# Optimization experiments

Measured on AMD Instinct MI355X. Metric: run time of the kernel, lower is better.

Reference implementation:

```python
import jax, jax.numpy as jnp
import numpy as np

D_MODEL = 1024
NUM_HEADS = 16


def setup_inputs() -> dict:
    key = jax.random.key(0)
    ks = jax.random.split(key, 5)
    scale = 1.0 / np.sqrt(D_MODEL)
    X = jax.random.normal(ks[0], (4, 2048, D_MODEL), dtype=jnp.float32)
    W_q = jax.random.normal(ks[1], (D_MODEL, D_MODEL), dtype=jnp.float32) * scale
    W_k = jax.random.normal(ks[2], (D_MODEL, D_MODEL), dtype=jnp.float32) * scale
    W_v = jax.random.normal(ks[3], (D_MODEL, D_MODEL), dtype=jnp.float32) * scale
    W_o = jax.random.normal(ks[4], (D_MODEL, D_MODEL), dtype=jnp.float32) * scale
    return {"X": X, "W_q": W_q, "W_k": W_k, "W_v": W_v, "W_o": W_o}


def reference(X, W_q, W_k, W_v, W_o):
    b, s, d_model = X.shape
    h = NUM_HEADS
    d_k = d_model // h
    # Linear projections (y = x @ W^T convention; W stored as [out,in] would be
    # x @ W.T, but with random weights we use x @ W — math is identical in form).
    def split_heads(y):
        return y.reshape(b, s, h, d_k).transpose(0, 2, 1, 3)  # b h s d
    q = split_heads(X @ W_q)
    k = split_heads(X @ W_k)
    v = split_heads(X @ W_v)
    scores = jnp.einsum('bhid,bhjd->bhij', q, k) / jnp.sqrt(jnp.float32(d_k))
    causal = jnp.tril(jnp.ones((s, s), dtype=bool))
    scores = jnp.where(causal[None, None], scores, jnp.float32(-jnp.inf))
    probs = jax.nn.softmax(scores, axis=-1)
    attended = jnp.einsum('bhij,bhjd->bhid', probs, v)
    out = attended.transpose(0, 2, 1, 3).reshape(b, s, d_model)
    return out @ W_o
```

## Files before the change

kernel.cpp:

```cpp
#include <hip/hip_runtime.h>

typedef __bf16 bf16;
typedef __attribute__((ext_vector_type(8))) __bf16 bf16x8;
typedef __attribute__((ext_vector_type(4))) float f32x4;
typedef __attribute__((ext_vector_type(16))) float f32x16;
typedef __attribute__((ext_vector_type(4))) unsigned short u16x4;
typedef __attribute__((ext_vector_type(2))) int v2i;

#define D_MODEL 1024
#define SEQ     2048
#define NB      4
#define NH      16
#define DK      64
#define MROWS   (NB * SEQ)

#define MFMA_BF16 __builtin_amdgcn_mfma_f32_16x16x32_bf16
#define MFMA32    __builtin_amdgcn_mfma_f32_32x32x16_bf16
#define EXP2F(x) __builtin_amdgcn_exp2f(x)
#define QSCALE 0.18033688011112042f

__device__ __forceinline__ bf16 f2b(float f) {
    union { float f; unsigned u; } c; c.f = f;
    unsigned r = (c.u + 0x7fffu + ((c.u >> 16) & 1u)) >> 16;
    union { unsigned short s; bf16 b; } o; o.s = (unsigned short)r;
    return o.b;
}
__device__ __forceinline__ unsigned short f2u(float f) {
    union { float f; unsigned u; } c; c.f = f;
    return (unsigned short)((c.u + 0x7fffu + ((c.u >> 16) & 1u)) >> 16);
}

__device__ __forceinline__ f32x16 zero16() {
    f32x16 z = {0.f,0.f,0.f,0.f,0.f,0.f,0.f,0.f,
                0.f,0.f,0.f,0.f,0.f,0.f,0.f,0.f};
    return z;
}

template <int N> struct IC { static constexpr int v = N; };

__global__ void prep_kernel(const float* __restrict__ X,
                            const float* __restrict__ Wq, const float* __restrict__ Wk,
                            const float* __restrict__ Wv, const float* __restrict__ Wo,
                            bf16* __restrict__ Xb, bf16* __restrict__ WqkvT,
                            bf16* __restrict__ WoT) {
    __shared__ float tile[32][33];
    const int bid = blockIdx.x;
    if (bid < 8192) {
        int i = bid * 256 + threadIdx.x;
        float4 v = ((const float4*)X)[i];
        u16x4 o; o[0] = f2u(v.x); o[1] = f2u(v.y); o[2] = f2u(v.z); o[3] = f2u(v.w);
        ((u16x4*)Xb)[i] = o;
    } else {
        int r = bid - 8192;
        int w = r >> 10, tl = r & 1023;
        const float* src = (w == 0) ? Wq : (w == 1) ? Wk : (w == 2) ? Wv : Wo;
        bf16* dst = (w == 3) ? WoT : WqkvT + (size_t)w * 1024 * 1024;
        const int n0 = (tl & 31) * 32, k0 = (tl >> 5) * 32;
        const int tx = threadIdx.x & 31, ty = threadIdx.x >> 5;
#pragma unroll
        for (int i = 0; i < 4; i++)
            tile[ty + i * 8][tx] = src[(size_t)(k0 + ty + i * 8) * 1024 + n0 + tx];
        __syncthreads();
#pragma unroll
        for (int i = 0; i < 4; i++)
            dst[(size_t)(n0 + ty + i * 8) * 1024 + k0 + tx] = f2b(tile[tx][ty + i * 8]);
    }
}

__global__ __launch_bounds__(256) void gemm_qkv(const bf16* __restrict__ A,
                                                const bf16* __restrict__ Bt,
                                                bf16* __restrict__ outQ,
                                                bf16* __restrict__ outV) {
    __shared__ __align__(16) bf16 lA[128 * 64];
    __shared__ __align__(16) bf16 lB[128 * 64];

    const int t = threadIdx.x;
    const int wid = t >> 6, lane = t & 63;
    const int ln = lane & 15, qd = lane >> 4;
    const int wm = wid >> 1, wn = wid & 1;

    const int bid = blockIdx.x;
    const int idx = bid >> 3;
    const int colb = (bid & 7) * 3 + (idx % 3);
    const int rowb = idx / 3;
    const int row0 = rowb * 128, col0 = colb * 128;
    const bool isQK = (col0 < 2048);

    const int srow = t >> 3;
    const int schunk = (t & 7) ^ (srow & 7);
    const bf16* ga = A  + (size_t)(row0 + srow) * 1024 + schunk * 8;
    const bf16* gb = Bt + (size_t)(col0 + srow) * 1024 + schunk * 8;
    const int swk = ln & 7;

    f32x4 acc[4][4];
#pragma unroll
    for (int i = 0; i < 4; i++)
#pragma unroll
        for (int j = 0; j < 4; j++) acc[i][j] = (f32x4){0.f, 0.f, 0.f, 0.f};

    for (int kb = 0; kb < 1024; kb += 64) {
#pragma unroll
        for (int c = 0; c < 4; c++) {
            __builtin_amdgcn_global_load_lds(
                (const __attribute__((address_space(1))) void*)(ga + kb + (size_t)c * 32 * 1024),
                (__attribute__((address_space(3))) void*)(&lA[t * 8 + c * 2048]), 16, 0, 0);
            __builtin_amdgcn_global_load_lds(
                (const __attribute__((address_space(1))) void*)(gb + kb + (size_t)c * 32 * 1024),
                (__attribute__((address_space(3))) void*)(&lB[t * 8 + c * 2048]), 16, 0, 0);
        }
        __syncthreads();

#pragma unroll
        for (int ks = 0; ks < 2; ks++) {
            bf16x8 af[4], bfr[4];
#pragma unroll
            for (int i = 0; i < 4; i++)
                af[i] = *(const bf16x8*)&lA[(wm * 64 + i * 16 + ln) * 64
                                            + ((ks * 4 + qd) ^ swk) * 8];
#pragma unroll
            for (int j = 0; j < 4; j++)
                bfr[j] = *(const bf16x8*)&lB[(wn * 64 + j * 16 + ln) * 64
                                             + ((ks * 4 + qd) ^ swk) * 8];
            if (isQK) {
#pragma unroll
                for (int i = 0; i < 4; i++)
#pragma unroll
                    for (int j = 0; j < 4; j++)
                        acc[i][j] = MFMA_BF16(bfr[j], af[i], acc[i][j], 0, 0, 0);
            } else {
#pragma unroll
                for (int i = 0; i < 4; i++)
#pragma unroll
                    for (int j = 0; j < 4; j++)
                        acc[i][j] = MFMA_BF16(af[i], bfr[j], acc[i][j], 0, 0, 0);
            }
        }
        __syncthreads();
    }

    if (isQK) {
#pragma unroll
        for (int i = 0; i < 4; i++)
#pragma unroll
            for (int j = 0; j < 4; j++) {
                int m  = row0 + wm * 64 + i * 16 + ln;
                int n0 = col0 + wn * 64 + j * 16 + qd * 4;
                float scale = (n0 < 1024) ? QSCALE : 1.0f;
                int b = m >> 11, s = m & 2047;
                int h = (n0 & 1023) >> 6, d0 = n0 & 63;
                size_t addr = (((size_t)(b * NH + h) * SEQ + s) * DK + d0)
                              + (size_t)(n0 >> 10) * 8388608;
                u16x4 w;
#pragma unroll
                for (int r = 0; r < 4; r++) w[r] = f2u(acc[i][j][r] * scale);
                *(u16x4*)&outQ[addr] = w;
            }
    } else {
#pragma unroll
        for (int i = 0; i < 4; i++)
#pragma unroll
            for (int j = 0; j < 4; j++) {
                int m0 = row0 + wm * 64 + i * 16 + qd * 4;
                int n  = col0 + wn * 64 + j * 16 + ln - 2048;
                int b = m0 >> 11, s0 = m0 & 2047;
                int h = n >> 6, d = n & 63;
                size_t addr = ((size_t)(b * NH + h) * DK + d) * SEQ + s0;
                u16x4 w;
#pragma unroll
                for (int r = 0; r < 4; r++) w[r] = f2u(acc[i][j][r]);
                *(u16x4*)&outV[addr] = w;
            }
    }
}

__global__ __launch_bounds__(256) void gemm_o(const bf16* __restrict__ A,
                                              const bf16* __restrict__ Bt,
                                              float* __restrict__ out) {
    __shared__ __align__(16) bf16 lA[128 * 64];
    __shared__ __align__(16) bf16 lB[128 * 64];

    const int t = threadIdx.x;
    const int wid = t >> 6, lane = t & 63;
    const int ln = lane & 15, qd = lane >> 4;
    const int wm = wid >> 1, wn = wid & 1;

    const int bid = blockIdx.x;
    const int colb = bid & 7, rowb = bid >> 3;
    const int row0 = rowb * 128, col0 = colb * 128;

    const int srow = t >> 3;
    const int schunk = (t & 7) ^ (srow & 7);
    const bf16* ga = A  + (size_t)(row0 + srow) * 1024 + schunk * 8;
    const bf16* gb = Bt + (size_t)(col0 + srow) * 1024 + schunk * 8;
    const int swk = ln & 7;

    f32x4 acc[4][4];
#pragma unroll
    for (int i = 0; i < 4; i++)
#pragma unroll
        for (int j = 0; j < 4; j++) acc[i][j] = (f32x4){0.f, 0.f, 0.f, 0.f};

    for (int kb = 0; kb < 1024; kb += 64) {
#pragma unroll
        for (int c = 0; c < 4; c++) {
            __builtin_amdgcn_global_load_lds(
                (const __attribute__((address_space(1))) void*)(ga + kb + (size_t)c * 32 * 1024),
                (__attribute__((address_space(3))) void*)(&lA[t * 8 + c * 2048]), 16, 0, 0);
            __builtin_amdgcn_global_load_lds(
                (const __attribute__((address_space(1))) void*)(gb + kb + (size_t)c * 32 * 1024),
                (__attribute__((address_space(3))) void*)(&lB[t * 8 + c * 2048]), 16, 0, 0);
        }
        __syncthreads();

#pragma unroll
        for (int ks = 0; ks < 2; ks++) {
            bf16x8 af[4], bfr[4];
#pragma unroll
            for (int i = 0; i < 4; i++)
                af[i] = *(const bf16x8*)&lA[(wm * 64 + i * 16 + ln) * 64
                                            + ((ks * 4 + qd) ^ swk) * 8];
#pragma unroll
            for (int j = 0; j < 4; j++)
                bfr[j] = *(const bf16x8*)&lB[(wn * 64 + j * 16 + ln) * 64
                                             + ((ks * 4 + qd) ^ swk) * 8];
#pragma unroll
            for (int i = 0; i < 4; i++)
#pragma unroll
                for (int j = 0; j < 4; j++)
                    acc[i][j] = MFMA_BF16(bfr[j], af[i], acc[i][j], 0, 0, 0);
        }
        __syncthreads();
    }

#pragma unroll
    for (int i = 0; i < 4; i++)
#pragma unroll
        for (int j = 0; j < 4; j++) {
            int m  = row0 + wm * 64 + i * 16 + ln;
            int n0 = col0 + wn * 64 + j * 16 + qd * 4;
            *(f32x4*)&out[(size_t)m * 1024 + n0] = acc[i][j];
        }
}

__global__ __launch_bounds__(256, 2) void attn_kernel(const bf16* __restrict__ Q,
                                                      const bf16* __restrict__ K,
                                                      const bf16* __restrict__ Vt,
                                                      bf16* __restrict__ attn_out) {
    __shared__ __align__(16) bf16 smem[4][64 * 64];

    const int t = threadIdx.x;
    const int wid = t >> 6, lane = t & 63;
    const int qcol = lane & 31, h = lane >> 5;

    const int bid = blockIdx.x;
    const int bh = ((bid >> 6) << 3) | (bid & 7);
    const int p  = (bid >> 3) & 7;
    const int gA = 15 - p, gB = p;
    const int ntA = 2 * gA + 2;

    const bf16* Qh = Q  + (size_t)bh * SEQ * DK;
    const bf16* Kh = K  + (size_t)bh * SEQ * DK;
    const bf16* Vh = Vt + (size_t)bh * DK * SEQ;

    const int srow = t >> 3;
    const int schunk = (t & 7) ^ (srow & 7);
    const bf16* kgp = Kh + (size_t)srow * DK + schunk * 8;
    const bf16* vgp = Vh + (size_t)srow * SEQ + schunk * 8;

    const char* sbase = (const char*)&smem[0][0];
    int raddr[4];
#pragma unroll
    for (int tt = 0; tt < 4; tt++)
        raddr[tt] = qcol * 128 + (((2 * tt + h) ^ (lane & 7)) * 16);

    int qw0;
    bf16x8 qf[4];
    f32x16 o[2];
    float l;

    auto initGroup = [&](int g) {
        qw0 = g * 128 + wid * 32;
#pragma unroll
        for (int tt = 0; tt < 4; tt++)
            qf[tt] = *(const bf16x8*)(Qh + (size_t)(qw0 + qcol) * DK + tt * 16 + h * 8);
        o[0] = zero16(); o[1] = zero16();
        l = 0.f;
    };

    const int b = bh >> 4, head = bh & 15;
    auto finalize = [&]() {
        float ll = l + __shfl_xor(l, 32);
        const float inv = 1.0f / ll;
        const size_t orow = ((size_t)(b * SEQ + qw0 + qcol)) * D_MODEL + head * DK;
#pragma unroll
        for (int m = 0; m < 2; m++)
#pragma unroll
            for (int q4 = 0; q4 < 4; q4++) {
                u16x4 w;
#pragma unroll
                for (int c = 0; c < 4; c++) w[c] = f2u(o[m][q4 * 4 + c] * inv);
                *(u16x4*)&attn_out[orow + m * 32 + q4 * 8 + h * 4] = w;
            }
    };

    auto stage = [&](int kb, int buf) {
#pragma unroll
        for (int c = 0; c < 2; c++) {
            __builtin_amdgcn_global_load_lds(
                (const __attribute__((address_space(1))) void*)(kgp + (size_t)(kb + c * 32) * DK),
                (__attribute__((address_space(3))) void*)(&smem[buf][t * 8 + c * 2048]), 16, 0, 0);
            __builtin_amdgcn_global_load_lds(
                (const __attribute__((address_space(1))) void*)(vgp + (size_t)c * 32 * SEQ + kb),
                (__attribute__((address_space(3))) void*)(&smem[2 + buf][t * 8 + c * 2048]), 16, 0, 0);
        }
    };

    auto qkt = [&](const char* kb_base) -> f32x16 {
        f32x16 z = zero16();
#pragma unroll
        for (int tt = 0; tt < 4; tt++) {
            bf16x8 kf = *(const bf16x8*)(kb_base + raddr[tt]);
            z = MFMA32(kf, qf[tt], z, 0, 0, 0);
        }
        return z;
    };

    auto pvks = [&](const f32x16& s, int b8, int ks, const char* vbase) {
        unsigned A, B, C, D;
        asm("v_cvt_pk_bf16_f32 %0, %1, %2"
            : "=v"(A) : "v"(s[b8 + 0]), "v"(s[b8 + 1]));
        asm("v_cvt_pk_bf16_f32 %0, %1, %2"
            : "=v"(B) : "v"(s[b8 + 2]), "v"(s[b8 + 3]));
        asm("v_cvt_pk_bf16_f32 %0, %1, %2"
            : "=v"(C) : "v"(s[b8 + 4]), "v"(s[b8 + 5]));
        asm("v_cvt_pk_bf16_f32 %0, %1, %2"
            : "=v"(D) : "v"(s[b8 + 6]), "v"(s[b8 + 7]));
        v2i r02 = __builtin_amdgcn_permlane32_swap((int)A, (int)C, false, false);
        v2i r13 = __builtin_amdgcn_permlane32_swap((int)B, (int)D, false, false);
        union { unsigned u[4]; bf16x8 v; } pf;
        pf.u[0] = (unsigned)r02[0];
        pf.u[1] = (unsigned)r13[0];
        pf.u[2] = (unsigned)r02[1];
        pf.u[3] = (unsigned)r13[1];
#pragma unroll
        for (int m = 0; m < 2; m++) {
            bf16x8 vf = *(const bf16x8*)(vbase + raddr[ks] + m * 4096);
            o[m] = MFMA32(vf, pf.v, o[m], 0, 0, 0);
        }
    };

    auto smaxFull = [&](f32x16& s) -> float {
#pragma unroll
        for (int r = 0; r < 16; r++) s[r] = EXP2F(s[r]);
        float s0 = (s[0] + s[1]) + (s[2] + s[3]);
        float s1 = (s[4] + s[5]) + (s[6] + s[7]);
        float s2 = (s[8] + s[9]) + (s[10] + s[11]);
        float s3 = (s[12] + s[13]) + (s[14] + s[15]);
        return (s0 + s1) + (s2 + s3);
    };

    auto compute = [&](auto curc, int kb) {
        constexpr int CUR = decltype(curc)::v;
        const char* kbase = sbase + CUR * 8192;
        const char* vbase = sbase + 16384 + CUR * 8192;
        const int rel = qw0 - kb;
        if (rel < 0) return;
        if (rel >= 64) {
            __builtin_amdgcn_s_setprio(1);
            f32x16 s0 = qkt(kbase);
            f32x16 s1 = qkt(kbase + 4096);
            __builtin_amdgcn_s_setprio(0);
            l += smaxFull(s0);
            __builtin_amdgcn_s_setprio(1);
            pvks(s0, 0, 0, vbase);
            pvks(s0, 8, 1, vbase);
            __builtin_amdgcn_s_setprio(0);
            l += smaxFull(s1);
            __builtin_amdgcn_s_setprio(1);
            pvks(s1, 0, 2, vbase);
            pvks(s1, 8, 3, vbase);
            __builtin_amdgcn_s_setprio(0);
        } else {
            const int nt = (rel >> 5) + 1;
            f32x16 st[2];
#pragma unroll
            for (int n = 0; n < 2; n++)
                if (n < nt) st[n] = qkt(kbase + n * 4096);
            float ps = 0.f;
#pragma unroll
            for (int n = 0; n < 2; n++)
                if (n < nt) {
                    const bool diag = (rel == 32 * n);
#pragma unroll
                    for (int r = 0; r < 16; r++) {
                        float pv = EXP2F(st[n][r]);
                        if (diag) {
                            const int kloc = (r & 3) + 8 * (r >> 2) + 4 * h;
                            pv = (kloc > qcol) ? 0.f : pv;
                        }
                        st[n][r] = pv;
                    }
                    float s0 = (st[n][0] + st[n][1]) + (st[n][2] + st[n][3]);
                    float s1 = (st[n][4] + st[n][5]) + (st[n][6] + st[n][7]);
                    float s2 = (st[n][8] + st[n][9]) + (st[n][10] + st[n][11]);
                    float s3 = (st[n][12] + st[n][13]) + (st[n][14] + st[n][15]);
                    ps += (s0 + s1) + (s2 + s3);
                }
            l += ps;
#pragma unroll
            for (int ks = 0; ks < 4; ks++)
                if (ks < 2 * nt)
                    pvks(st[ks >> 1], (ks & 1) * 8, ks, vbase);
        }
    };

    auto step = [&](auto curc, int i) {
        constexpr int CUR = decltype(curc)::v;
        __syncthreads();
        const int nx = i + 1;
        if (nx < 34) {
            const int tnx = (nx < ntA) ? nx : nx - ntA;
            stage(tnx * 64, CUR ^ 1);
        }
        const int kb = ((i < ntA) ? i : i - ntA) * 64;
        compute(curc, kb);
        if (i == ntA - 1) { finalize(); initGroup(gB); }
    };

    stage(0, 0);
    initGroup(gA);

    step(IC<0>{}, 0);
#pragma unroll 1
    for (int ii = 0; ii < 16; ii++) {
        step(IC<1>{}, 2 * ii + 1);
        step(IC<0>{}, 2 * ii + 2);
    }
    step(IC<1>{}, 33);
    finalize();
}

extern "C" void kernel_launch(void* const* d_in, const int* in_sizes, int n_in,
                              void* d_out, int out_size, void* d_ws, size_t ws_size,
                              hipStream_t stream) {
    const float* X  = (const float*)d_in[0];
    const float* Wq = (const float*)d_in[1];
    const float* Wk = (const float*)d_in[2];
    const float* Wv = (const float*)d_in[3];
    const float* Wo = (const float*)d_in[4];
    float* out = (float*)d_out;
    char* ws = (char*)d_ws;

    bf16* Xb    = (bf16*)(ws);
    bf16* WqkvT = (bf16*)(ws + (16u << 20));
    bf16* WoT   = (bf16*)(ws + (22u << 20));
    bf16* Qb    = (bf16*)(ws + (24u << 20));
    bf16* Vt    = (bf16*)(ws + (56u << 20));
    bf16* Attn  = Xb;
    bf16* Kb    = Qb + (size_t)8388608;

    prep_kernel<<<dim3(12288), dim3(256), 0, stream>>>(X, Wq, Wk, Wv, Wo,
                                                       Xb, WqkvT, WoT);

    gemm_qkv<<<dim3(1536), dim3(256), 0, stream>>>(Xb, WqkvT, Qb, Vt);

    attn_kernel<<<dim3(512), dim3(256), 0, stream>>>(Qb, Kb, Vt, Attn);

    gemm_o<<<dim3(512), dim3(256), 0, stream>>>(Attn, WoT, out);
}
```

Baseline: 234.3 us.

## Double attention K/V tile depth to 128 keys per stage, vectorize weight transpose stores

The attention kernel now stages 128 keys per double-buffered step instead of 64. This halves the number of __syncthreads barriers and stage issues across the KV loop, and the shared-memory buffers grow to 64 KB. The 128-key tile is processed as two 64-key halves, with the causal mask handled per half. Separately, the weight-transpose kernel now writes four packed bf16 values per thread as a single 8-byte store instead of four scalar stores. The larger LDS footprint may limit occupancy below the two-blocks-per-CU launch bound, and the diagonal block may now load keys that go unused.

```diff
diff --git a/kernel.cpp b/kernel.cpp
--- a/kernel.cpp
+++ b/kernel.cpp
@@ -61,9 +61,12 @@
         for (int i = 0; i < 4; i++)
             tile[ty + i * 8][tx] = src[(size_t)(k0 + ty + i * 8) * 1024 + n0 + tx];
         __syncthreads();
-#pragma unroll
-        for (int i = 0; i < 4; i++)
-            dst[(size_t)(n0 + ty + i * 8) * 1024 + k0 + tx] = f2b(tile[tx][ty + i * 8]);
+        const int n4 = threadIdx.x >> 3;
+        const int k4 = (threadIdx.x & 7) * 4;
+        u16x4 ww;
+#pragma unroll
+        for (int j = 0; j < 4; j++) ww[j] = f2u(tile[k4 + j][n4]);
+        *(u16x4*)&dst[(size_t)(n0 + n4) * 1024 + k0 + k4] = ww;
     }
 }
 
@@ -246,7 +249,7 @@
                                                       const bf16* __restrict__ K,
                                                       const bf16* __restrict__ Vt,
                                                       bf16* __restrict__ attn_out) {
-    __shared__ __align__(16) bf16 smem[4][64 * 64];
+    __shared__ __align__(16) bf16 smem[4][128 * 64];
 
     const int t = threadIdx.x;
     const int wid = t >> 6, lane = t & 63;
@@ -256,7 +259,7 @@
     const int bh = ((bid >> 6) << 3) | (bid & 7);
     const int p  = (bid >> 3) & 7;
     const int gA = 15 - p, gB = p;
-    const int ntA = 2 * gA + 2;
+    const int ntA = gA + 1;
 
     const bf16* Qh = Q  + (size_t)bh * SEQ * DK;
     const bf16* Kh = K  + (size_t)bh * SEQ * DK;
@@ -305,14 +308,19 @@
 
     auto stage = [&](int kb, int buf) {
 #pragma unroll
-        for (int c = 0; c < 2; c++) {
+        for (int c = 0; c < 4; c++)
             __builtin_amdgcn_global_load_lds(
                 (const __attribute__((address_space(1))) void*)(kgp + (size_t)(kb + c * 32) * DK),
                 (__attribute__((address_space(3))) void*)(&smem[buf][t * 8 + c * 2048]), 16, 0, 0);
-            __builtin_amdgcn_global_load_lds(
-                (const __attribute__((address_space(1))) void*)(vgp + (size_t)c * 32 * SEQ + kb),
-                (__attribute__((address_space(3))) void*)(&smem[2 + buf][t * 8 + c * 2048]), 16, 0, 0);
-        }
+#pragma unroll
+        for (int hh = 0; hh < 2; hh++)
+#pragma unroll
+            for (int c = 0; c < 2; c++)
+                __builtin_amdgcn_global_load_lds(
+                    (const __attribute__((address_space(1))) void*)
+                        (vgp + (size_t)c * 32 * SEQ + kb + hh * 64),
+                    (__attribute__((address_space(3))) void*)
+                        (&smem[2 + buf][t * 8 + hh * 4096 + c * 2048]), 16, 0, 0);
     };
 
     auto qkt = [&](const char* kb_base) -> f32x16 {
@@ -361,56 +369,61 @@
 
     auto compute = [&](auto curc, int kb) {
         constexpr int CUR = decltype(curc)::v;
-        const char* kbase = sbase + CUR * 8192;
-        const char* vbase = sbase + 16384 + CUR * 8192;
-        const int rel = qw0 - kb;
-        if (rel < 0) return;
-        if (rel >= 64) {
-            __builtin_amdgcn_s_setprio(1);
-            f32x16 s0 = qkt(kbase);
-            f32x16 s1 = qkt(kbase + 4096);
-            __builtin_amdgcn_s_setprio(0);
-            l += smaxFull(s0);
-            __builtin_amdgcn_s_setprio(1);
-            pvks(s0, 0, 0, vbase);
-            pvks(s0, 8, 1, vbase);
-            __builtin_amdgcn_s_setprio(0);
-            l += smaxFull(s1);
-            __builtin_amdgcn_s_setprio(1);
-            pvks(s1, 0, 2, vbase);
-            pvks(s1, 8, 3, vbase);
-            __builtin_amdgcn_s_setprio(0);
-        } else {
-            const int nt = (rel >> 5) + 1;
-            f32x16 st[2];
-#pragma unroll
-            for (int n = 0; n < 2; n++)
-                if (n < nt) st[n] = qkt(kbase + n * 4096);
-            float ps = 0.f;
-#pragma unroll
-            for (int n = 0; n < 2; n++)
-                if (n < nt) {
-                    const bool diag = (rel == 32 * n);
-#pragma unroll
-                    for (int r = 0; r < 16; r++) {
-                        float pv = EXP2F(st[n][r]);
-                        if (diag) {
-                            const int kloc = (r & 3) + 8 * (r >> 2) + 4 * h;
-                            pv = (kloc > qcol) ? 0.f : pv;
+        const char* kT = sbase + CUR * 16384;
+        const char* vT = sbase + 32768 + CUR * 16384;
+#pragma unroll
+        for (int half = 0; half < 2; half++) {
+            const char* kbase = kT + half * 8192;
+            const char* vbase = vT + half * 8192;
+            const int rel = qw0 - (kb + half * 64);
+            if (rel < 0) continue;
+            if (rel >= 64) {
+                __builtin_amdgcn_s_setprio(1);
+                f32x16 s0 = qkt(kbase);
+                f32x16 s1 = qkt(kbase + 4096);
+                __builtin_amdgcn_s_setprio(0);
+                l += smaxFull(s0);
+                __builtin_amdgcn_s_setprio(1);
+                pvks(s0, 0, 0, vbase);
+                pvks(s0, 8, 1, vbase);
+                __builtin_amdgcn_s_setprio(0);
+                l += smaxFull(s1);
+                __builtin_amdgcn_s_setprio(1);
+                pvks(s1, 0, 2, vbase);
+                pvks(s1, 8, 3, vbase);
+                __builtin_amdgcn_s_setprio(0);
+            } else {
+                const int nt = (rel >> 5) + 1;
+                f32x16 st[2];
+#pragma unroll
+                for (int n = 0; n < 2; n++)
+                    if (n < nt) st[n] = qkt(kbase + n * 4096);
+                float ps = 0.f;
+#pragma unroll
+                for (int n = 0; n < 2; n++)
+                    if (n < nt) {
+                        const bool diag = (rel == 32 * n);
+#pragma unroll
+                        for (int r = 0; r < 16; r++) {
+                            float pv = EXP2F(st[n][r]);
+                            if (diag) {
+                                const int kloc = (r & 3) + 8 * (r >> 2) + 4 * h;
+                                pv = (kloc > qcol) ? 0.f : pv;
+                            }
+                            st[n][r] = pv;
                         }
-                        st[n][r] = pv;
+                        float s0 = (st[n][0] + st[n][1]) + (st[n][2] + st[n][3]);
+                        float s1 = (st[n][4] + st[n][5]) + (st[n][6] + st[n][7]);
+                        float s2 = (st[n][8] + st[n][9]) + (st[n][10] + st[n][11]);
+                        float s3 = (st[n][12] + st[n][13]) + (st[n][14] + st[n][15]);
+                        ps += (s0 + s1) + (s2 + s3);
                     }
-                    float s0 = (st[n][0] + st[n][1]) + (st[n][2] + st[n][3]);
-                    float s1 = (st[n][4] + st[n][5]) + (st[n][6] + st[n][7]);
-                    float s2 = (st[n][8] + st[n][9]) + (st[n][10] + st[n][11]);
-                    float s3 = (st[n][12] + st[n][13]) + (st[n][14] + st[n][15]);
-                    ps += (s0 + s1) + (s2 + s3);
-                }
-            l += ps;
-#pragma unroll
-            for (int ks = 0; ks < 4; ks++)
-                if (ks < 2 * nt)
-                    pvks(st[ks >> 1], (ks & 1) * 8, ks, vbase);
+                l += ps;
+#pragma unroll
+                for (int ks = 0; ks < 4; ks++)
+                    if (ks < 2 * nt)
+                        pvks(st[ks >> 1], (ks & 1) * 8, ks, vbase);
+            }
         }
     };
 
@@ -418,11 +431,11 @@
         constexpr int CUR = decltype(curc)::v;
         __syncthreads();
         const int nx = i + 1;
-        if (nx < 34) {
+        if (nx < 17) {
             const int tnx = (nx < ntA) ? nx : nx - ntA;
-            stage(tnx * 64, CUR ^ 1);
-        }
-        const int kb = ((i < ntA) ? i : i - ntA) * 64;
+            stage(tnx * 128, CUR ^ 1);
+        }
+        const int kb = ((i < ntA) ? i : i - ntA) * 128;
         compute(curc, kb);
         if (i == ntA - 1) { finalize(); initGroup(gB); }
     };
@@ -432,11 +445,10 @@
 
     step(IC<0>{}, 0);
 #pragma unroll 1
-    for (int ii = 0; ii < 16; ii++) {
+    for (int ii = 0; ii < 8; ii++) {
         step(IC<1>{}, 2 * ii + 1);
         step(IC<0>{}, 2 * ii + 2);
     }
-    step(IC<1>{}, 33);
     finalize();
 }
 
```

Result: no change. 234.1 us (-0.1%).

## Split paired causal attention groups into separate blocks and vectorize weight transpose stores

Applied to the files above, without the earlier changes.

The attention kernel no longer pairs a heavy and a light query group per block to balance causal work. Each block now handles one 128-row query group with a variable number of key steps, and the grid doubles to 1024 blocks with launch bounds raised to 4 blocks per CU. The intent is more parallelism and occupancy, relying on the hardware scheduler to balance the uneven blocks, at the risk of register pressure and tail imbalance. The prep kernel's transpose now writes four bf16 values per thread as one 8-byte store instead of four scalar stores.

```diff
diff --git a/kernel.cpp b/kernel.cpp
--- a/kernel.cpp
+++ b/kernel.cpp
@@ -61,9 +61,12 @@
         for (int i = 0; i < 4; i++)
             tile[ty + i * 8][tx] = src[(size_t)(k0 + ty + i * 8) * 1024 + n0 + tx];
         __syncthreads();
-#pragma unroll
-        for (int i = 0; i < 4; i++)
-            dst[(size_t)(n0 + ty + i * 8) * 1024 + k0 + tx] = f2b(tile[tx][ty + i * 8]);
+        const int n4 = threadIdx.x >> 3;
+        const int k4 = (threadIdx.x & 7) * 4;
+        u16x4 ww;
+#pragma unroll
+        for (int j = 0; j < 4; j++) ww[j] = f2u(tile[k4 + j][n4]);
+        *(u16x4*)&dst[(size_t)(n0 + n4) * 1024 + k0 + k4] = ww;
     }
 }
 
@@ -242,7 +245,7 @@
         }
 }
 
-__global__ __launch_bounds__(256, 2) void attn_kernel(const bf16* __restrict__ Q,
+__global__ __launch_bounds__(256, 4) void attn_kernel(const bf16* __restrict__ Q,
                                                       const bf16* __restrict__ K,
                                                       const bf16* __restrict__ Vt,
                                                       bf16* __restrict__ attn_out) {
@@ -253,10 +256,9 @@
     const int qcol = lane & 31, h = lane >> 5;
 
     const int bid = blockIdx.x;
-    const int bh = ((bid >> 6) << 3) | (bid & 7);
-    const int p  = (bid >> 3) & 7;
-    const int gA = 15 - p, gB = p;
-    const int ntA = 2 * gA + 2;
+    const int bh = ((bid >> 7) << 3) | (bid & 7);
+    const int g  = 15 - ((bid >> 3) & 15);
+    const int nsteps = 2 * g + 2;
 
     const bf16* Qh = Q  + (size_t)bh * SEQ * DK;
     const bf16* Kh = K  + (size_t)bh * SEQ * DK;
@@ -273,35 +275,16 @@
     for (int tt = 0; tt < 4; tt++)
         raddr[tt] = qcol * 128 + (((2 * tt + h) ^ (lane & 7)) * 16);
 
-    int qw0;
+    const int qw0 = g * 128 + wid * 32;
+
     bf16x8 qf[4];
+#pragma unroll
+    for (int tt = 0; tt < 4; tt++)
+        qf[tt] = *(const bf16x8*)(Qh + (size_t)(qw0 + qcol) * DK + tt * 16 + h * 8);
+
     f32x16 o[2];
-    float l;
-
-    auto initGroup = [&](int g) {
-        qw0 = g * 128 + wid * 32;
-#pragma unroll
-        for (int tt = 0; tt < 4; tt++)
-            qf[tt] = *(const bf16x8*)(Qh + (size_t)(qw0 + qcol) * DK + tt * 16 + h * 8);
-        o[0] = zero16(); o[1] = zero16();
-        l = 0.f;
-    };
-
-    const int b = bh >> 4, head = bh & 15;
-    auto finalize = [&]() {
-        float ll = l + __shfl_xor(l, 32);
-        const float inv = 1.0f / ll;
-        const size_t orow = ((size_t)(b * SEQ + qw0 + qcol)) * D_MODEL + head * DK;
-#pragma unroll
-        for (int m = 0; m < 2; m++)
-#pragma unroll
-            for (int q4 = 0; q4 < 4; q4++) {
-                u16x4 w;
-#pragma unroll
-                for (int c = 0; c < 4; c++) w[c] = f2u(o[m][q4 * 4 + c] * inv);
-                *(u16x4*)&attn_out[orow + m * 32 + q4 * 8 + h * 4] = w;
-            }
-    };
+    o[0] = zero16(); o[1] = zero16();
+    float l = 0.f;
 
     auto stage = [&](int kb, int buf) {
 #pragma unroll
@@ -418,26 +401,33 @@
         constexpr int CUR = decltype(curc)::v;
         __syncthreads();
         const int nx = i + 1;
-        if (nx < 34) {
-            const int tnx = (nx < ntA) ? nx : nx - ntA;
-            stage(tnx * 64, CUR ^ 1);
-        }
-        const int kb = ((i < ntA) ? i : i - ntA) * 64;
-        compute(curc, kb);
-        if (i == ntA - 1) { finalize(); initGroup(gB); }
+        if (nx < nsteps) stage(nx * 64, CUR ^ 1);
+        compute(curc, i * 64);
     };
 
     stage(0, 0);
-    initGroup(gA);
 
     step(IC<0>{}, 0);
 #pragma unroll 1
-    for (int ii = 0; ii < 16; ii++) {
+    for (int ii = 0; ii < g; ii++) {
         step(IC<1>{}, 2 * ii + 1);
         step(IC<0>{}, 2 * ii + 2);
     }
-    step(IC<1>{}, 33);
-    finalize();
+    step(IC<1>{}, 2 * g + 1);
+
+    l += __shfl_xor(l, 32);
+    const float inv = 1.0f / l;
+    const int b = bh >> 4, head = bh & 15;
+    const size_t orow = ((size_t)(b * SEQ + qw0 + qcol)) * D_MODEL + head * DK;
+#pragma unroll
+    for (int m = 0; m < 2; m++)
+#pragma unroll
+        for (int q4 = 0; q4 < 4; q4++) {
+            u16x4 w;
+#pragma unroll
+            for (int c = 0; c < 4; c++) w[c] = f2u(o[m][q4 * 4 + c] * inv);
+            *(u16x4*)&attn_out[orow + m * 32 + q4 * 8 + h * 4] = w;
+        }
 }
 
 extern "C" void kernel_launch(void* const* d_in, const int* in_sizes, int n_in,
@@ -464,7 +454,7 @@
 
     gemm_qkv<<<dim3(1536), dim3(256), 0, stream>>>(Xb, WqkvT, Qb, Vt);
 
-    attn_kernel<<<dim3(512), dim3(256), 0, stream>>>(Qb, Kb, Vt, Attn);
+    attn_kernel<<<dim3(1024), dim3(256), 0, stream>>>(Qb, Kb, Vt, Attn);
 
     gemm_o<<<dim3(512), dim3(256), 0, stream>>>(Attn, WoT, out);
 }
```

New measurement: 254.6 us. 8.7% more time.
